# Kernel tuning notes

Measured on AMD Instinct MI355X. Metric: run time of the kernel, lower is better.

The kernel has to match this reference:

```python
import jax, jax.numpy as jnp
import numpy as np

N_MEMORY = 128
INPUT_LEN = 512
OUTPUT_LEN = 256
N_FRAMES = 65536


def setup_inputs() -> dict:
    key = jax.random.key(0)
    k1, k2, k3, k4, k5 = jax.random.split(key, 5)
    return {
        "inputs": jax.random.normal(k1, (INPUT_LEN, N_FRAMES), dtype=jnp.float32),
        "W1": jax.random.normal(k2, (2 * N_MEMORY, INPUT_LEN), dtype=jnp.float32) * 0.05,
        "B1": jax.random.normal(k3, (2 * N_MEMORY, 1), dtype=jnp.float32) * 0.05,
        "W2": jax.random.normal(k4, (OUTPUT_LEN, N_MEMORY), dtype=jnp.float32) * 0.05,
        "B2": jax.random.normal(k5, (OUTPUT_LEN, 1), dtype=jnp.float32) * 0.05,
    }


def reference(inputs, W1, B1, W2, B2):
    # h: (2M, T)
    h = jax.nn.sigmoid(jnp.matmul(W1, inputs) + B1)
    M = W1.shape[0] // 2
    left, right = h[:M], h[M:]          # each (M, T)
    prod = left * right                  # gate product, (M, T)

    # Linear recurrence: u_0 = 0; u_t = prod[:, t-1] * u_{t-1} + (1 - left[:, t-1])
    # Affine pairs for t = 1..T-1, time-major: (T-1, M)
    a = prod[:, :-1].T
    b = (1.0 - left[:, :-1]).T

    def combine(c1, c2):
        a1, b1 = c1
        a2, b2 = c2
        return a1 * a2, a2 * b1 + b2

    _, bb = jax.lax.associative_scan(combine, (a, b))
    # u_0 = 0 => u_t = bb_t; prepend the zero initial state as column 0
    z = jnp.concatenate([jnp.zeros((M, 1), dtype=inputs.dtype), bb.T], axis=1)  # (M, T)

    out = 1.0 - jax.nn.sigmoid(jnp.matmul(W2, z) + B2)  # (output_len, T)
    return out
```

## Files before the change

kernel.cpp:

```cpp
#include <hip/hip_runtime.h>

typedef unsigned short u16;
typedef short bf16x8 __attribute__((ext_vector_type(8)));
typedef float f32x4 __attribute__((ext_vector_type(4)));

#define NF 65536
#define GCH 512

__device__ __forceinline__ float sigm(float x){ return 1.0f/(1.0f+__expf(-x)); }

__device__ __forceinline__ u16 f2bf(float f){
  union { float f; unsigned u; } v; v.f = f;
  unsigned r = (v.u + 0x7fffu + ((v.u >> 16) & 1u)) >> 16;
  return (u16)r;
}

#define AS1(p) ((const __attribute__((address_space(1))) unsigned int*)(p))
#define AS3(p) ((__attribute__((address_space(3))) unsigned int*)(p))

__global__ __launch_bounds__(256) void k_prep(const float* __restrict__ W1, const float* __restrict__ W2,
                                              u16* __restrict__ W1f, u16* __restrict__ W2f){
  int idx = blockIdx.x*256 + threadIdx.x;
  {
    int j  = idx & 7;
    int L  = (idx >> 3) & 63;
    int ks = (idx >> 9) & 1;
    int rt = (idx >> 10) & 15;
    int ck = idx >> 14;
    int row = 16*rt + (L & 15);
    int k   = ck*64 + ks*32 + ((L >> 4) << 3) + j;
    W1f[idx] = f2bf(W1[row*512 + k]);
  }
  if (idx < 32768){
    int j  = idx & 7;
    int L  = (idx >> 3) & 63;
    int ks = (idx >> 9) & 3;
    int rt = idx >> 11;
    int row = 16*rt + (L & 15);
    int m   = ks*32 + ((L >> 4) << 3) + j;
    W2f[idx] = f2bf(W2[row*128 + m]);
  }
}

__global__ __launch_bounds__(256) void k_tr(const float* __restrict__ x, u16* __restrict__ xT){
  __shared__ float ls[64*65];
  const int tid = threadIdx.x;
  const int bt = blockIdx.x & 1023, bk = blockIdx.x >> 10;
  const int T0 = bt*64, K0 = bk*64;
  #pragma unroll
  for (int l=0;l<4;l++){
    int idx = tid + l*256;
    int kl = idx >> 4, c4 = idx & 15;
    float4 v = *(const float4*)(x + (size_t)(K0+kl)*NF + T0 + c4*4);
    float* d = ls + kl*65 + c4*4;
    d[0]=v.x; d[1]=v.y; d[2]=v.z; d[3]=v.w;
  }
  __syncthreads();
  #pragma unroll
  for (int l=0;l<2;l++){
    int p = tid + l*256;
    int t = p >> 3, kb = p & 7;
    unsigned u[8];
    #pragma unroll
    for (int m=0;m<8;m++) u[m] = f2bf(ls[(kb*8+m)*65 + t]);
    uint4 pk;
    pk.x = u[0] | (u[1]<<16); pk.y = u[2] | (u[3]<<16);
    pk.z = u[4] | (u[5]<<16); pk.w = u[6] | (u[7]<<16);
    *(uint4*)(xT + (size_t)(T0+t)*512 + K0 + kb*8) = pk;
  }
}

__global__ __launch_bounds__(256, 2) void k_gemm1(const u16* __restrict__ xT,
        const u16* __restrict__ W1f, const float* __restrict__ B1,
        float* __restrict__ Aa, float* __restrict__ Bb){
  __shared__ __align__(16) u16 ws[16384];
  __shared__ __align__(16) u16 xs[8192];
  const int tid = threadIdx.x;
  const int wv = tid >> 6, L = tid & 63;
  const int q = L >> 4, ln = L & 15;
  const int F0 = blockIdx.x * 128;
  const int rt0 = 2*wv;

  f32x4 acc[4][8];
  #pragma unroll
  for (int a=0;a<4;a++)
    #pragma unroll
    for (int c=0;c<8;c++) acc[a][c] = (f32x4){0.f,0.f,0.f,0.f};

  for (int ck=0; ck<8; ++ck){
    #pragma unroll
    for (int i=0;i<8;i++){
      int s = wv*8 + i;
      __builtin_amdgcn_global_load_lds(AS1(W1f + ck*16384 + s*512 + L*8), AS3(ws + s*512), 16, 0, 0);
    }
    #pragma unroll
    for (int i=0;i<4;i++){
      int s = wv*4 + i;
      int c = s >> 1, ks = s & 1;
      int t = F0 + c*16 + ln;
      int k = ck*64 + ks*32 + q*8;
      __builtin_amdgcn_global_load_lds(AS1(xT + (size_t)t*512 + k), AS3(xs + s*512), 16, 0, 0);
    }
    __syncthreads();
    #pragma unroll
    for (int ks=0; ks<2; ++ks){
      bf16x8 af[4];
      af[0] = ((const bf16x8*)ws)[( rt0   *2+ks)*64 + L];
      af[1] = ((const bf16x8*)ws)[((rt0+1)*2+ks)*64 + L];
      af[2] = ((const bf16x8*)ws)[((rt0+8)*2+ks)*64 + L];
      af[3] = ((const bf16x8*)ws)[((rt0+9)*2+ks)*64 + L];
      #pragma unroll
      for (int c=0;c<8;c++){
        bf16x8 bf = ((const bf16x8*)xs)[(c*2+ks)*64 + L];
        acc[0][c] = __builtin_amdgcn_mfma_f32_16x16x32_bf16(af[0], bf, acc[0][c], 0,0,0);
        acc[1][c] = __builtin_amdgcn_mfma_f32_16x16x32_bf16(af[1], bf, acc[1][c], 0,0,0);
        acc[2][c] = __builtin_amdgcn_mfma_f32_16x16x32_bf16(af[2], bf, acc[2][c], 0,0,0);
        acc[3][c] = __builtin_amdgcn_mfma_f32_16x16x32_bf16(af[3], bf, acc[3][c], 0,0,0);
      }
    }
    __syncthreads();
  }
  #pragma unroll
  for (int pr=0; pr<2; ++pr){
    int mb = 32*wv + 16*pr + 4*q;
    float bl[4], br[4];
    #pragma unroll
    for (int r=0;r<4;r++){ bl[r] = B1[mb+r]; br[r] = B1[mb+128+r]; }
    #pragma unroll
    for (int c=0;c<8;c++){
      int t = F0 + 16*c + ln;
      f32x4 Lv = acc[pr][c], Rv = acc[pr+2][c];
      float a4[4], b4[4];
      #pragma unroll
      for (int r=0;r<4;r++){
        float le = sigm(Lv[r] + bl[r]);
        float ri = sigm(Rv[r] + br[r]);
        a4[r] = le*ri; b4[r] = 1.0f - le;
      }
      *(float4*)(Aa + (size_t)t*128 + mb) = make_float4(a4[0],a4[1],a4[2],a4[3]);
      *(float4*)(Bb + (size_t)t*128 + mb) = make_float4(b4[0],b4[1],b4[2],b4[3]);
    }
  }
}

__global__ __launch_bounds__(128) void k_red(const float* __restrict__ Aa, const float* __restrict__ Bb,
                                             float* __restrict__ Ac, float* __restrict__ Bc){
  const int m = threadIdx.x, g = blockIdx.x;
  const float* ap = Aa + (size_t)g*128*128 + m;
  const float* bp = Bb + (size_t)g*128*128 + m;
  float A = 1.f, B = 0.f;
  #pragma unroll 8
  for (int t=0;t<128;t++){
    float a = ap[(size_t)t*128], b = bp[(size_t)t*128];
    B = fmaf(a, B, b);
    A *= a;
  }
  Ac[g*128+m] = A;
  Bc[g*128+m] = B;
}

__global__ __launch_bounds__(128) void k_scan(const float* __restrict__ Ac, const float* __restrict__ Bc,
                                              float* __restrict__ Pb){
  const int m = threadIdx.x;
  float B = 0.f;
  #pragma unroll 8
  for (int g=0; g<GCH; ++g){
    Pb[g*128+m] = B;
    B = fmaf(Ac[g*128+m], B, Bc[g*128+m]);
  }
}

__global__ __launch_bounds__(512, 2) void k_apply(const float* __restrict__ Aa, const float* __restrict__ Bb,
        const float* __restrict__ Pb, const u16* __restrict__ W2f, const float* __restrict__ B2,
        float* __restrict__ out){
  __shared__ __align__(16) u16 zf[16384];
  const int tid = threadIdx.x;
  const int g = blockIdx.x, T0 = g*128;

  if (tid < 128){
    const int m = tid;
    float s = Pb[g*128 + m];
    const float* ap = Aa + (size_t)T0*128 + m;
    const float* bp = Bb + (size_t)T0*128 + m;
    const int base_m = (m>>5)*512 + ((m>>3)&3)*128 + (m&7);
    #pragma unroll 4
    for (int t=0;t<128;t++){
      zf[base_m + (t>>4)*2048 + (t&15)*8] = f2bf(s);
      s = fmaf(ap[(size_t)t*128], s, bp[(size_t)t*128]);
    }
  }
  __syncthreads();

  const int wv = tid >> 6, L = tid & 63;
  const int q = L >> 4, ln = L & 15;
  f32x4 acc[2][8];
  #pragma unroll
  for (int a=0;a<2;a++)
    #pragma unroll
    for (int c=0;c<8;c++) acc[a][c] = (f32x4){0.f,0.f,0.f,0.f};

  #pragma unroll
  for (int ks=0; ks<4; ++ks){
    bf16x8 af0 = ((const bf16x8*)W2f)[((2*wv  )*4+ks)*64 + L];
    bf16x8 af1 = ((const bf16x8*)W2f)[((2*wv+1)*4+ks)*64 + L];
    #pragma unroll
    for (int c=0;c<8;c++){
      bf16x8 bf = ((const bf16x8*)zf)[(c*4+ks)*64 + L];
      acc[0][c] = __builtin_amdgcn_mfma_f32_16x16x32_bf16(af0, bf, acc[0][c], 0,0,0);
      acc[1][c] = __builtin_amdgcn_mfma_f32_16x16x32_bf16(af1, bf, acc[1][c], 0,0,0);
    }
  }

  #pragma unroll
  for (int rs=0;rs<2;rs++){
    int rowb = (2*wv+rs)*16 + q*4;
    float b2[4];
    #pragma unroll
    for (int r=0;r<4;r++) b2[r] = B2[rowb+r];
    #pragma unroll
    for (int c=0;c<8;c++){
      int t = T0 + 16*c + ln;
      #pragma unroll
      for (int r=0;r<4;r++)
        out[(size_t)(rowb+r)*NF + t] = sigm(-(acc[rs][c][r] + b2[r]));
    }
  }
}

extern "C" void kernel_launch(void* const* d_in, const int* in_sizes, int n_in,
                              void* d_out, int out_size, void* d_ws, size_t ws_size,
                              hipStream_t stream) {
  const float* x  = (const float*)d_in[0];
  const float* W1 = (const float*)d_in[1];
  const float* B1 = (const float*)d_in[2];
  const float* W2 = (const float*)d_in[3];
  const float* B2 = (const float*)d_in[4];
  float* out = (float*)d_out;

  u16*   W1f = (u16*)d_ws;
  u16*   W2f = W1f + 131072;
  float* Aa  = (float*)d_ws + 81920;
  float* Bb  = Aa + (size_t)NF*128;
  float* Ac  = Bb + (size_t)NF*128;
  float* Bc  = Ac + (size_t)GCH*128;
  float* Pb  = Bc + (size_t)GCH*128;
  u16*   xT  = (u16*)d_out;

  k_prep <<<512, 256, 0, stream>>>(W1, W2, W1f, W2f);
  k_tr   <<<8192, 256, 0, stream>>>(x, xT);
  k_gemm1<<<512, 256, 0, stream>>>(xT, W1f, B1, Aa, Bb);
  k_red  <<<GCH, 128, 0, stream>>>(Aa, Bb, Ac, Bc);
  k_scan <<<1, 128, 0, stream>>>(Ac, Bc, Pb);
  k_apply<<<GCH, 512, 0, stream>>>(Aa, Bb, Pb, W2f, B2, out);
}
```

Measured before the change: 339.7 us.

## Fuse chunk reduction into GEMM epilogue and parallelize scan stages

```diff
diff --git a/kernel.cpp b/kernel.cpp
--- a/kernel.cpp
+++ b/kernel.cpp
@@ -72,13 +72,15 @@
 
 __global__ __launch_bounds__(256, 2) void k_gemm1(const u16* __restrict__ xT,
         const u16* __restrict__ W1f, const float* __restrict__ B1,
-        float* __restrict__ Aa, float* __restrict__ Bb){
+        float* __restrict__ Aa, float* __restrict__ Bb,
+        float* __restrict__ Ac, float* __restrict__ Bc){
   __shared__ __align__(16) u16 ws[16384];
   __shared__ __align__(16) u16 xs[8192];
   const int tid = threadIdx.x;
   const int wv = tid >> 6, L = tid & 63;
   const int q = L >> 4, ln = L & 15;
-  const int F0 = blockIdx.x * 128;
+  const int g = blockIdx.x;
+  const int F0 = g * 128;
   const int rt0 = 2*wv;
 
   f32x4 acc[4][8];
@@ -126,6 +128,7 @@
     float bl[4], br[4];
     #pragma unroll
     for (int r=0;r<4;r++){ bl[r] = B1[mb+r]; br[r] = B1[mb+128+r]; }
+    float RA[4], RB[4];
     #pragma unroll
     for (int c=0;c<8;c++){
       int t = F0 + 16*c + ln;
@@ -139,34 +142,52 @@
       }
       *(float4*)(Aa + (size_t)t*128 + mb) = make_float4(a4[0],a4[1],a4[2],a4[3]);
       *(float4*)(Bb + (size_t)t*128 + mb) = make_float4(b4[0],b4[1],b4[2],b4[3]);
-    }
-  }
-}
-
-__global__ __launch_bounds__(128) void k_red(const float* __restrict__ Aa, const float* __restrict__ Bb,
-                                             float* __restrict__ Ac, float* __restrict__ Bc){
-  const int m = threadIdx.x, g = blockIdx.x;
-  const float* ap = Aa + (size_t)g*128*128 + m;
-  const float* bp = Bb + (size_t)g*128*128 + m;
+      #pragma unroll
+      for (int r=0;r<4;r++){
+        float As = a4[r], Bs = b4[r];
+        #pragma unroll
+        for (int d=1; d<16; d<<=1){
+          float Ap = __shfl_xor(As, d);
+          float Bp = __shfl_xor(Bs, d);
+          Bs = (ln & d) ? fmaf(As, Bp, Bs) : fmaf(Ap, Bs, Bp);
+          As *= Ap;
+        }
+        if (c == 0){ RA[r] = As; RB[r] = Bs; }
+        else       { RB[r] = fmaf(As, RB[r], Bs); RA[r] *= As; }
+      }
+    }
+    if (ln == 0){
+      #pragma unroll
+      for (int r=0;r<4;r++){
+        Ac[g*128 + mb + r] = RA[r];
+        Bc[g*128 + mb + r] = RB[r];
+      }
+    }
+  }
+}
+
+__global__ __launch_bounds__(1024) void k_scan(const float* __restrict__ Ac, const float* __restrict__ Bc,
+                                               float* __restrict__ Pb){
+  __shared__ float sA[8][128], sB[8][128];
+  const int tid = threadIdx.x;
+  const int m = tid & 127, s = tid >> 7;
+  const int g0 = s*64;
   float A = 1.f, B = 0.f;
-  #pragma unroll 8
-  for (int t=0;t<128;t++){
-    float a = ap[(size_t)t*128], b = bp[(size_t)t*128];
+  #pragma unroll 16
+  for (int i=0;i<64;i++){
+    float a = Ac[(g0+i)*128 + m], b = Bc[(g0+i)*128 + m];
     B = fmaf(a, B, b);
     A *= a;
   }
-  Ac[g*128+m] = A;
-  Bc[g*128+m] = B;
-}
-
-__global__ __launch_bounds__(128) void k_scan(const float* __restrict__ Ac, const float* __restrict__ Bc,
-                                              float* __restrict__ Pb){
-  const int m = threadIdx.x;
-  float B = 0.f;
-  #pragma unroll 8
-  for (int g=0; g<GCH; ++g){
-    Pb[g*128+m] = B;
-    B = fmaf(Ac[g*128+m], B, Bc[g*128+m]);
+  sA[s][m] = A; sB[s][m] = B;
+  __syncthreads();
+  float v = 0.f;
+  for (int s2=0; s2<s; ++s2) v = fmaf(sA[s2][m], v, sB[s2][m]);
+  #pragma unroll 16
+  for (int i=0;i<64;i++){
+    int g = g0+i;
+    Pb[g*128+m] = v;
+    v = fmaf(Ac[g*128+m], v, Bc[g*128+m]);
   }
 }
 
@@ -174,19 +195,30 @@
         const float* __restrict__ Pb, const u16* __restrict__ W2f, const float* __restrict__ B2,
         float* __restrict__ out){
   __shared__ __align__(16) u16 zf[16384];
+  __shared__ float sA[4][128], sB[4][128];
   const int tid = threadIdx.x;
   const int g = blockIdx.x, T0 = g*128;
 
-  if (tid < 128){
-    const int m = tid;
-    float s = Pb[g*128 + m];
-    const float* ap = Aa + (size_t)T0*128 + m;
-    const float* bp = Bb + (size_t)T0*128 + m;
+  {
+    const int m = tid & 127, s4 = tid >> 7;
+    const float* ap = Aa + (size_t)(T0 + s4*32)*128 + m;
+    const float* bp = Bb + (size_t)(T0 + s4*32)*128 + m;
+    float areg[32], breg[32];
+    #pragma unroll
+    for (int i=0;i<32;i++){ areg[i] = ap[(size_t)i*128]; breg[i] = bp[(size_t)i*128]; }
+    float A = 1.f, Bv = 0.f;
+    #pragma unroll
+    for (int i=0;i<32;i++){ Bv = fmaf(areg[i], Bv, breg[i]); A *= areg[i]; }
+    sA[s4][m] = A; sB[s4][m] = Bv;
+    __syncthreads();
+    float v = Pb[g*128 + m];
+    for (int s2=0; s2<s4; ++s2) v = fmaf(sA[s2][m], v, sB[s2][m]);
     const int base_m = (m>>5)*512 + ((m>>3)&3)*128 + (m&7);
-    #pragma unroll 4
-    for (int t=0;t<128;t++){
-      zf[base_m + (t>>4)*2048 + (t&15)*8] = f2bf(s);
-      s = fmaf(ap[(size_t)t*128], s, bp[(size_t)t*128]);
+    #pragma unroll
+    for (int i=0;i<32;i++){
+      int t = s4*32 + i;
+      zf[base_m + (t>>4)*2048 + (t&15)*8] = f2bf(v);
+      v = fmaf(areg[i], v, breg[i]);
     }
   }
   __syncthreads();
@@ -248,8 +280,7 @@
 
   k_prep <<<512, 256, 0, stream>>>(W1, W2, W1f, W2f);
   k_tr   <<<8192, 256, 0, stream>>>(x, xT);
-  k_gemm1<<<512, 256, 0, stream>>>(xT, W1f, B1, Aa, Bb);
-  k_red  <<<GCH, 128, 0, stream>>>(Aa, Bb, Ac, Bc);
-  k_scan <<<1, 128, 0, stream>>>(Ac, Bc, Pb);
+  k_gemm1<<<512, 256, 0, stream>>>(xT, W1f, B1, Aa, Bb, Ac, Bc);
+  k_scan <<<1, 1024, 0, stream>>>(Ac, Bc, Pb);
   k_apply<<<GCH, 512, 0, stream>>>(Aa, Bb, Pb, W2f, B2, out);
 }
```

Measured after the change: 338.3 us. About the same (-0.4%).
